# Kernel tuning notes

Hardware: AMD Instinct MI355X
Metric: run time of the kernel (lower is better)

Reference implementation:

```python
import jax, jax.numpy as jnp
import numpy as np

D = 128
N = 50000    # nodes in bond graph g
E = 500000   # edges in g == nodes in line graph lg
ELG = 500000 # edges in line graph lg


def _linear_params(key, d_in, d_out):
    k1, k2 = jax.random.split(key)
    s = 1.0 / np.sqrt(d_in)
    W = jax.random.uniform(k1, (d_in, d_out), jnp.float32, -s, s)
    b = jax.random.uniform(k2, (d_out,), jnp.float32, -s, s)
    return W, b


def setup_inputs() -> dict:
    key = jax.random.key(0)
    ks = jax.random.split(key, 32)
    inp = {
        'x': jax.random.normal(ks[0], (N, D), jnp.float32),
        'edge_x': jax.random.normal(ks[1], (E, D), jnp.float32),
        'lg_edge_attr': jax.random.normal(ks[2], (ELG, D), jnp.float32),
        'g_edge_index': jax.random.randint(ks[3], (2, E), 0, N),
        'lg_edge_index': jax.random.randint(ks[4], (2, ELG), 0, E),
    }
    i = 5
    for pre in ('eu', 'nu'):
        for nm in ('sg', 'dg', 'eg', 'su', 'du'):
            W, b = _linear_params(ks[i], D, D); i += 1
            inp[pre + '_W' + nm] = W
            inp[pre + '_b' + nm] = b
        inp[pre + '_gamma'] = jnp.ones((D,), jnp.float32)
        inp[pre + '_beta'] = jnp.zeros((D,), jnp.float32)
    return inp


def _layernorm(x, g, b):
    m = jnp.mean(x, -1, keepdims=True)
    v = jnp.var(x, -1, keepdims=True)
    return (x - m) * jax.lax.rsqrt(v + 1e-5) * g + b


def _egc(x, edge_index, edge_attr,
         Wsg, bsg, Wdg, bdg, Weg, beg, Wsu, bsu, Wdu, bdu, gamma, beta):
    # Edge-gated graph conv. PyG convention: x_i = x[dst], x_j = x[src],
    # aggregate messages at dst (edge_index[1]).
    src, dst = edge_index[0], edge_index[1]
    # Project once at node level, then gather (same math as gather-then-linear).
    sg = x @ Wsg + bsg          # src_gate(x_i) precomputed per node
    dg = x @ Wdg + bdg          # dst_gate(x_j)
    du = x @ Wdu + bdu          # dst_update(x_j)
    gate = jax.nn.silu(sg[dst] + dg[src] + edge_attr @ Weg + beg)  # [E, D]
    msg = gate * du[src]                                           # [E, D]
    aggr = jax.ops.segment_sum(msg, dst, num_segments=x.shape[0])  # [N, D]
    out = jax.nn.silu(_layernorm(x @ Wsu + bsu + aggr, gamma, beta))
    return out + x  # residual (in_channels == out_channels here)


def reference(x, edge_x, lg_edge_attr,
              eu_Wsg, eu_bsg, eu_Wdg, eu_bdg, eu_Weg, eu_beg,
              eu_Wsu, eu_bsu, eu_Wdu, eu_bdu, eu_gamma, eu_beta,
              nu_Wsg, nu_bsg, nu_Wdg, nu_bdg, nu_Weg, nu_beg,
              nu_Wsu, nu_bsu, nu_Wdu, nu_bdu, nu_gamma, nu_beta,
              g_edge_index, lg_edge_index):
    # 1) edge update on line graph (lg nodes are g's edges)
    ea = _egc(edge_x, lg_edge_index, lg_edge_attr,
              eu_Wsg, eu_bsg, eu_Wdg, eu_bdg, eu_Weg, eu_beg,
              eu_Wsu, eu_bsu, eu_Wdu, eu_bdu, eu_gamma, eu_beta)
    # 2) node update on bond graph using updated edge features
    xn = _egc(x, g_edge_index, ea,
              nu_Wsg, nu_bsg, nu_Wdg, nu_bdg, nu_Weg, nu_beg,
              nu_Wsu, nu_bsu, nu_Wdu, nu_bdu, nu_gamma, nu_beta)
    return (xn, ea)
```

## Files before the change

kernel.cpp:

```cpp
#include <hip/hip_runtime.h>
#include <stdint.h>

#define DD 128
#define WPAD 72

typedef __bf16 bf16x8 __attribute__((ext_vector_type(8)));
typedef float f32x4 __attribute__((ext_vector_type(4)));
typedef unsigned short u16;
typedef u16 u16x8 __attribute__((ext_vector_type(8)));

__device__ __forceinline__ u16 f2bf(float f) {
  union { __bf16 h; u16 u; } v; v.h = (__bf16)f; return v.u;
}
__device__ __forceinline__ float bf2f(u16 b) {
  union { uint32_t u; float f; } v; v.u = (uint32_t)b << 16; return v.f;
}
__device__ __forceinline__ float silu_f(float x) {
  return x / (1.0f + __expf(-x));
}
__device__ __forceinline__ uint32_t pkbf(float lo, float hi) {
  return (uint32_t)f2bf(lo) | ((uint32_t)f2bf(hi) << 16);
}

struct ARegs { f32x4 v[8][2]; };

__device__ __forceinline__ void issue_A(ARegs& r, const float* __restrict__ src,
                                        int base, int M, int tid) {
#pragma unroll
  for (int i = 0; i < 8; ++i) {
    int id = tid + (i << 8);
    int row = id >> 4;
    int cc = id & 15;
    if (base + row < M) {
      const f32x4* p = (const f32x4*)(src + (size_t)(base + row) * DD + cc * 8);
      r.v[i][0] = p[0];
      r.v[i][1] = p[1];
    } else {
      r.v[i][0] = (f32x4){0.f, 0.f, 0.f, 0.f};
      r.v[i][1] = (f32x4){0.f, 0.f, 0.f, 0.f};
    }
  }
}

__device__ __forceinline__ void write_A(u16* Ab, const ARegs& r, int tid) {
#pragma unroll
  for (int i = 0; i < 8; ++i) {
    int id = tid + (i << 8);
    int row = id >> 4;
    int cc = id & 15;
    u16x8 o;
    o[0] = f2bf(r.v[i][0][0]); o[1] = f2bf(r.v[i][0][1]);
    o[2] = f2bf(r.v[i][0][2]); o[3] = f2bf(r.v[i][0][3]);
    o[4] = f2bf(r.v[i][1][0]); o[5] = f2bf(r.v[i][1][1]);
    o[6] = f2bf(r.v[i][1][2]); o[7] = f2bf(r.v[i][1][3]);
    *(u16x8*)&Ab[row * DD + ((cc ^ (row & 7)) << 3)] = o;
  }
}

struct BRegs { bf16x8 b[4][4]; };

__device__ __forceinline__ void load_B(BRegs& br, const u16* __restrict__ wt,
                                       int lane, int wc) {
  int g = lane >> 4, r15 = lane & 15;
  const u16* wbase = wt + (size_t)(wc * 64 + r15) * DD;
#pragma unroll
  for (int kk = 0; kk < 4; ++kk) {
    int ko = ((kk << 2) | g) << 3;
#pragma unroll
    for (int n = 0; n < 4; ++n)
      br.b[kk][n] = *(const bf16x8*)&wbase[n * 16 * DD + ko];
  }
}

__device__ __forceinline__ void mma_stage(const u16* Ab, const BRegs& br,
                                          f32x4 acc[4][4], int lane, int wr) {
  int g = lane >> 4, r15 = lane & 15, s = r15 & 7;
#pragma unroll
  for (int kk = 0; kk < 4; ++kk) {
    bf16x8 af[4];
#pragma unroll
    for (int m = 0; m < 4; ++m) {
      int rr = wr * 64 + m * 16 + r15;
      af[m] = *(const bf16x8*)&Ab[rr * DD + ((((kk << 2) | g) ^ s) << 3)];
    }
#pragma unroll
    for (int m = 0; m < 4; ++m)
#pragma unroll
      for (int n = 0; n < 4; ++n)
        acc[m][n] = __builtin_amdgcn_mfma_f32_16x16x32_bf16(af[m], br.b[kk][n], acc[m][n], 0, 0, 0);
  }
}

__device__ __forceinline__ void init_acc(f32x4 a[4][4], const float* __restrict__ bias,
                                         int lane, int wc) {
  int l15 = lane & 15;
#pragma unroll
  for (int n = 0; n < 4; ++n) {
    float b = bias ? bias[wc * 64 + n * 16 + l15] : 0.f;
    f32x4 v = {b, b, b, b};
#pragma unroll
    for (int m = 0; m < 4; ++m) a[m][n] = v;
  }
}

__device__ __forceinline__ void store_lds_wave(const f32x4 acc[4][4], u16* wb,
                                               int lane) {
  int l15 = lane & 15;
  bool oddl = lane & 1;
#pragma unroll
  for (int m = 0; m < 4; ++m) {
    int rb = m * 16 + ((lane >> 4) << 2);
#pragma unroll
    for (int j = 0; j < 4; ++j) {
      int row = rb + j;
#pragma unroll
      for (int n0 = 0; n0 < 4; n0 += 2) {
        int c0 = n0 * 16 + l15;
        float v0 = acc[m][n0][j];
        float v1 = acc[m][n0 + 1][j];
        float t0 = __shfl_xor(v0, 1);
        float t1 = __shfl_xor(v1, 1);
        uint32_t pk = oddl ? pkbf(t1, v1) : pkbf(v0, t0);
        int col2 = oddl ? (c0 + 15) : c0;
        *(uint32_t*)&wb[row * WPAD + col2] = pk;
      }
    }
  }
}

__device__ __forceinline__ void copy_out_wave(const u16* wb, u16* __restrict__ out,
                                              size_t rs, int co, int base, int M,
                                              int lane, int wr, int wc,
                                              const int* sPerm) {
  int lr8 = lane >> 3;
  int lc = (lane & 7) * 8;
#pragma unroll
  for (int p = 0; p < 8; ++p) {
    int lrow = p * 8 + lr8;
    int row = wr * 64 + lrow;
    if (base + row < M) {
      int orow = sPerm ? sPerm[row] : (base + row);
      u16x8 v = *(const u16x8*)&wb[lrow * WPAD + lc];
      *(u16x8*)&out[(size_t)orow * rs + co + wc * 64 + lc] = v;
    }
  }
}

__device__ __forceinline__ void proj_four_body(
    int M, int base, const float* __restrict__ src, const u16* __restrict__ wt,
    const float* __restrict__ bF, u16* __restrict__ o_sg,
    u16* __restrict__ o_dgdu, u16* __restrict__ o_su, u16* Ab, u16* Wb) {
  int tid = threadIdx.x, lane = tid & 63, wid = tid >> 6;
  int wr = wid >> 1, wc = wid & 1;
  BRegs b0, b1;
  {
    ARegs ar;
    issue_A(ar, src, base, M, tid);
    load_B(b0, wt + 0 * 16384, lane, wc);
    write_A(Ab, ar, tid);
  }
  __syncthreads();
  u16* wb = Wb + wid * (64 * WPAD);
  f32x4 acc[4][4];
  init_acc(acc, bF, lane, wc);
  mma_stage(Ab, b0, acc, lane, wr);
  load_B(b1, wt + 1 * 16384, lane, wc);
  store_lds_wave(acc, wb, lane);
  copy_out_wave(wb, o_sg, DD, 0, base, M, lane, wr, wc, nullptr);
  init_acc(acc, nullptr, lane, wc);
  mma_stage(Ab, b1, acc, lane, wr);
  load_B(b0, wt + 3 * 16384, lane, wc);
  store_lds_wave(acc, wb, lane);
  copy_out_wave(wb, o_dgdu, 2 * DD, 0, base, M, lane, wr, wc, nullptr);
  init_acc(acc, bF + 128, lane, wc);
  mma_stage(Ab, b0, acc, lane, wr);
  load_B(b1, wt + 4 * 16384, lane, wc);
  store_lds_wave(acc, wb, lane);
  copy_out_wave(wb, o_dgdu, 2 * DD, DD, base, M, lane, wr, wc, nullptr);
  init_acc(acc, bF + 256, lane, wc);
  mma_stage(Ab, b1, acc, lane, wr);
  store_lds_wave(acc, wb, lane);
  copy_out_wave(wb, o_su, DD, 0, base, M, lane, wr, wc, nullptr);
}

__device__ __forceinline__ void proj_one_body(
    int M, int base, const float* __restrict__ src, const u16* __restrict__ wt,
    const int* __restrict__ perm, u16* __restrict__ o,
    u16* Ab, u16* Wb, int* sPerm) {
  int tid = threadIdx.x, lane = tid & 63, wid = tid >> 6;
  int wr = wid >> 1, wc = wid & 1;
  BRegs b0;
  {
    ARegs ar;
    issue_A(ar, src, base, M, tid);
    if (perm && tid < 128)
      sPerm[tid] = (base + tid < M) ? perm[base + tid] : 0;
    load_B(b0, wt, lane, wc);
    write_A(Ab, ar, tid);
  }
  __syncthreads();
  u16* wb = Wb + wid * (64 * WPAD);
  f32x4 acc[4][4];
  init_acc(acc, nullptr, lane, wc);
  mma_stage(Ab, b0, acc, lane, wr);
  store_lds_wave(acc, wb, lane);
  copy_out_wave(wb, o, DD, 0, base, M, lane, wr, wc, perm ? sPerm : nullptr);
}

__global__ void __launch_bounds__(256, 2) proj_mega(
    int gE, int gLG,
    int E, const float* __restrict__ ex, const u16* __restrict__ wtE,
    const float* __restrict__ bFE,
    u16* __restrict__ sgE, u16* __restrict__ dgduE, u16* __restrict__ suE,
    int ELG, const float* __restrict__ lga, const u16* __restrict__ wtLG,
    const int* __restrict__ permE, u16* __restrict__ egp,
    int N, const float* __restrict__ x, const u16* __restrict__ wtN,
    const float* __restrict__ bFN,
    u16* __restrict__ sgN, u16* __restrict__ dgduN, u16* __restrict__ suN) {
  __shared__ u16 Ab[128 * DD];
  __shared__ u16 Wb[4 * 64 * WPAD];
  __shared__ int sPerm[128];
  int b = blockIdx.x;
  if (b < gE)
    proj_four_body(E, b * 128, ex, wtE, bFE, sgE, dgduE, suE, Ab, Wb);
  else if (b < gE + gLG)
    proj_one_body(ELG, (b - gE) * 128, lga, wtLG, permE, egp, Ab, Wb, sPerm);
  else
    proj_four_body(N, (b - gE - gLG) * 128, x, wtN, bFN, sgN, dgduN, suN, Ab, Wb);
}

__global__ void __launch_bounds__(256, 2) proj_single(
    int M, const float* __restrict__ src, const u16* __restrict__ wt,
    const int* __restrict__ perm, u16* __restrict__ o) {
  __shared__ u16 Ab[128 * DD];
  __shared__ u16 Wb[4 * 64 * WPAD];
  __shared__ int sPerm[128];
  proj_one_body(M, blockIdx.x * 128, src, wt, perm, o, Ab, Wb, sPerm);
}

__global__ void __launch_bounds__(256) hist_kernel(const int* __restrict__ dst,
                                                   int Me, int* __restrict__ cnt) {
  int i = blockIdx.x * blockDim.x + threadIdx.x;
  if (i < Me) atomicAdd(&cnt[dst[i]], 1);
}

__global__ void __launch_bounds__(256) scan1_kernel(const int* __restrict__ cnt, int M,
                                                    int* __restrict__ out,
                                                    int* __restrict__ bsum) {
  __shared__ int sh[256];
  int t = threadIdx.x;
  int i0 = blockIdx.x * 1024 + t * 4;
  int v[4];
#pragma unroll
  for (int k = 0; k < 4; ++k) v[k] = (i0 + k < M) ? cnt[i0 + k] : 0;
  int s = v[0] + v[1] + v[2] + v[3];
  sh[t] = s;
  __syncthreads();
#pragma unroll
  for (int off = 1; off < 256; off <<= 1) {
    int x = (t >= off) ? sh[t - off] : 0;
    __syncthreads();
    sh[t] += x;
    __syncthreads();
  }
  int run = sh[t] - s;
  if (t == 255) bsum[blockIdx.x] = sh[255];
#pragma unroll
  for (int k = 0; k < 4; ++k) {
    if (i0 + k < M) out[i0 + k] = run;
    run += v[k];
  }
}

__global__ void __launch_bounds__(256) scan2_kernel(int* __restrict__ bsum, int NB) {
  __shared__ int sh[512];
  int t = threadIdx.x;
  for (int i = t; i < 512; i += 256) sh[i] = (i < NB) ? bsum[i] : 0;
  __syncthreads();
  for (int off = 1; off < 512; off <<= 1) {
    int tmp[2];
#pragma unroll
    for (int q = 0; q < 2; ++q) {
      int i = t + q * 256;
      tmp[q] = (i >= off) ? sh[i - off] : 0;
    }
    __syncthreads();
#pragma unroll
    for (int q = 0; q < 2; ++q) sh[t + q * 256] += tmp[q];
    __syncthreads();
  }
  for (int i = t; i < NB; i += 256) bsum[i] = (i == 0) ? 0 : sh[i - 1];
}

__global__ void __launch_bounds__(256) scan3_kernel(int* __restrict__ rowptr,
                                                    const int* __restrict__ bscan,
                                                    int M, int Medges,
                                                    int* __restrict__ head) {
  int i = blockIdx.x * blockDim.x + threadIdx.x;
  if (i < M) {
    int v = rowptr[i] + bscan[i >> 10];
    rowptr[i] = v;
    head[i] = v;
  }
  if (i == 0) rowptr[M] = Medges;
}

__global__ void __launch_bounds__(256) eid_kernel(const int* __restrict__ src,
                                                  const int* __restrict__ dst, int Me,
                                                  int* __restrict__ head,
                                                  int* __restrict__ srcs,
                                                  int* __restrict__ pos) {
  int i = blockIdx.x * blockDim.x + threadIdx.x;
  if (i < Me) {
    int s = atomicAdd(&head[dst[i]], 1);
    srcs[s] = src[i];
    pos[i] = s;
  }
}

__global__ void prep_weights(const float* __restrict__ w0, const float* __restrict__ w1,
                             const float* __restrict__ w2, const float* __restrict__ w3,
                             const float* __restrict__ w4, const float* __restrict__ w5,
                             const float* __restrict__ w6, const float* __restrict__ w7,
                             const float* __restrict__ w8, const float* __restrict__ w9,
                             u16* __restrict__ wt) {
  const float* W;
  switch (blockIdx.x) {
    case 0: W = w0; break; case 1: W = w1; break; case 2: W = w2; break;
    case 3: W = w3; break; case 4: W = w4; break; case 5: W = w5; break;
    case 6: W = w6; break; case 7: W = w7; break; case 8: W = w8; break;
    default: W = w9; break;
  }
  u16* dst = wt + blockIdx.x * 16384;
  for (int o = threadIdx.x; o < 16384; o += 256) {
    int n = o >> 7, k = o & 127;
    dst[o] = f2bf(W[k * DD + n]);
  }
}

__global__ void fold_bias(const float* __restrict__ e_sg, const float* __restrict__ e_dg,
                          const float* __restrict__ e_eg, const float* __restrict__ e_du,
                          const float* __restrict__ e_su,
                          const float* __restrict__ n_sg, const float* __restrict__ n_dg,
                          const float* __restrict__ n_eg, const float* __restrict__ n_du,
                          const float* __restrict__ n_su, float* __restrict__ out) {
  int i = threadIdx.x;
  if (i < 128) {
    out[i]        = e_sg[i] + e_dg[i] + e_eg[i];
    out[128 + i]  = e_du[i];
    out[256 + i]  = e_su[i];
    out[384 + i]  = n_sg[i] + n_dg[i] + n_eg[i];
    out[512 + i]  = n_du[i];
    out[640 + i]  = n_su[i];
  }
}

__global__ void __launch_bounds__(256) gfin_kernel(
    int M, const int* __restrict__ rptr,
    const int* __restrict__ srcs,
    const u16* __restrict__ sg_t, const u16* __restrict__ dgdu_t,
    const u16* __restrict__ su_t, const u16* __restrict__ egp,
    const float* __restrict__ gamma, const float* __restrict__ beta,
    const float* __restrict__ resid, float* __restrict__ out) {
  int gtid = blockIdx.x * blockDim.x + threadIdx.x;
  int r = gtid >> 4;
  int l16 = gtid & 15;
  if (r >= M) return;
  int c = l16 * 8;

  u16x8 sgp = *(const u16x8*)&sg_t[(size_t)r * DD + c];
  float sg[8], ax[8];
#pragma unroll
  for (int k = 0; k < 8; ++k) { sg[k] = bf2f(sgp[k]); ax[k] = 0.f; }

  int segb = rptr[r], sege = rptr[r + 1];
  for (int s = segb; s < sege; ++s) {
    int sv = srcs[s];
    u16x8 gp = *(const u16x8*)&egp[(size_t)s * DD + c];
    u16x8 dgp = *(const u16x8*)&dgdu_t[(size_t)sv * (2 * DD) + c];
    u16x8 dup = *(const u16x8*)&dgdu_t[(size_t)sv * (2 * DD) + DD + c];
#pragma unroll
    for (int k = 0; k < 8; ++k) {
      float g = silu_f(sg[k] + bf2f(dgp[k]) + bf2f(gp[k]));
      ax[k] += g * bf2f(dup[k]);
    }
  }

  u16x8 sup = *(const u16x8*)&su_t[(size_t)r * DD + c];
  float v[8];
  float sum = 0.f;
#pragma unroll
  for (int k = 0; k < 8; ++k) { v[k] = bf2f(sup[k]) + ax[k]; sum += v[k]; }
#pragma unroll
  for (int off = 1; off <= 8; off <<= 1) sum += __shfl_xor(sum, off);
  float mean = sum * (1.0f / 128.0f);
  float sq = 0.f;
#pragma unroll
  for (int k = 0; k < 8; ++k) { v[k] -= mean; sq += v[k] * v[k]; }
#pragma unroll
  for (int off = 1; off <= 8; off <<= 1) sq += __shfl_xor(sq, off);
  float rs = rsqrtf(sq * (1.0f / 128.0f) + 1e-5f);

  float4 gm0 = *(const float4*)&gamma[c];
  float4 gm1 = *(const float4*)&gamma[c + 4];
  float4 bt0 = *(const float4*)&beta[c];
  float4 bt1 = *(const float4*)&beta[c + 4];
  float4 rr0 = *(const float4*)&resid[(size_t)r * DD + c];
  float4 rr1 = *(const float4*)&resid[(size_t)r * DD + c + 4];
  float gmv[8] = {gm0.x, gm0.y, gm0.z, gm0.w, gm1.x, gm1.y, gm1.z, gm1.w};
  float btv[8] = {bt0.x, bt0.y, bt0.z, bt0.w, bt1.x, bt1.y, bt1.z, bt1.w};
  float rrv[8] = {rr0.x, rr0.y, rr0.z, rr0.w, rr1.x, rr1.y, rr1.z, rr1.w};
  float o[8];
#pragma unroll
  for (int k = 0; k < 8; ++k)
    o[k] = silu_f(v[k] * rs * gmv[k] + btv[k]) + rrv[k];
  float4 o0 = {o[0], o[1], o[2], o[3]};
  float4 o1 = {o[4], o[5], o[6], o[7]};
  *(float4*)&out[(size_t)r * DD + c] = o0;
  *(float4*)&out[(size_t)r * DD + c + 4] = o1;
}

extern "C" void kernel_launch(void* const* d_in, const int* in_sizes, int n_in,
                              void* d_out, int out_size, void* d_ws, size_t ws_size,
                              hipStream_t stream) {
  const float* x   = (const float*)d_in[0];
  const float* ex  = (const float*)d_in[1];
  const float* lga = (const float*)d_in[2];
  const int* gei   = (const int*)d_in[3];
  const int* lgei  = (const int*)d_in[4];
  int N   = in_sizes[0] / DD;
  int E   = in_sizes[3] / 2;
  int ELG = in_sizes[4] / 2;

  char* p = (char*)d_ws;
  size_t off = 0;
  auto alloc = [&](size_t bytes) { char* q = p + off; off += (bytes + 255) & ~255ull; return q; };

  u16* wt     = (u16*)alloc((size_t)10 * 16384 * 2);
  float* biasF = (float*)alloc(768 * 4);
  u16* sgE    = (u16*)alloc((size_t)E * DD * 2);
  u16* dgduE  = (u16*)alloc((size_t)E * 2 * DD * 2);
  u16* suE    = (u16*)alloc((size_t)E * DD * 2);
  int  maxME  = (ELG > E) ? ELG : E;
  u16* egpB   = (u16*)alloc((size_t)maxME * DD * 2);
  u16* sgN    = (u16*)alloc((size_t)N * DD * 2);
  u16* dgduN  = (u16*)alloc((size_t)N * 2 * DD * 2);
  u16* suN    = (u16*)alloc((size_t)N * DD * 2);
  int* cnt_e  = (int*)alloc((size_t)E * 4);
  int* rptr_e = (int*)alloc((size_t)(E + 1) * 4);
  int* head_e = (int*)alloc((size_t)E * 4);
  int* srcs_e = (int*)alloc((size_t)ELG * 4);
  int* pos_e  = (int*)alloc((size_t)ELG * 4);
  int* cnt_n  = (int*)alloc((size_t)N * 4);
  int* rptr_n = (int*)alloc((size_t)(N + 1) * 4);
  int* head_n = (int*)alloc((size_t)N * 4);
  int* srcs_n = (int*)alloc((size_t)E * 4);
  int* pos_n  = (int*)alloc((size_t)E * 4);
  int* bsum   = (int*)alloc(512 * 4);
  if (ws_size < off) return;

  float* xn_out = (float*)d_out;
  float* ea_out = (float*)d_out + (size_t)N * DD;

  prep_weights<<<10, 256, 0, stream>>>(
      (const float*)d_in[5], (const float*)d_in[7], (const float*)d_in[9],
      (const float*)d_in[13], (const float*)d_in[11],
      (const float*)d_in[17], (const float*)d_in[19], (const float*)d_in[21],
      (const float*)d_in[25], (const float*)d_in[23], wt);
  fold_bias<<<1, 128, 0, stream>>>(
      (const float*)d_in[6], (const float*)d_in[8], (const float*)d_in[10],
      (const float*)d_in[14], (const float*)d_in[12],
      (const float*)d_in[18], (const float*)d_in[20], (const float*)d_in[22],
      (const float*)d_in[26], (const float*)d_in[24], biasF);

  hipMemsetAsync(cnt_e, 0, (size_t)E * 4, stream);
  hipMemsetAsync(cnt_n, 0, (size_t)N * 4, stream);
  hist_kernel<<<(ELG + 255) / 256, 256, 0, stream>>>(lgei + ELG, ELG, cnt_e);
  hist_kernel<<<(E + 255) / 256, 256, 0, stream>>>(gei + E, E, cnt_n);

  int NBe = (E + 1023) / 1024;
  scan1_kernel<<<NBe, 256, 0, stream>>>(cnt_e, E, rptr_e, bsum);
  scan2_kernel<<<1, 256, 0, stream>>>(bsum, NBe);
  scan3_kernel<<<(E + 255) / 256, 256, 0, stream>>>(rptr_e, bsum, E, ELG, head_e);
  eid_kernel<<<(ELG + 255) / 256, 256, 0, stream>>>(lgei, lgei + ELG, ELG, head_e,
                                                    srcs_e, pos_e);

  int NBn = (N + 1023) / 1024;
  scan1_kernel<<<NBn, 256, 0, stream>>>(cnt_n, N, rptr_n, bsum);
  scan2_kernel<<<1, 256, 0, stream>>>(bsum, NBn);
  scan3_kernel<<<(N + 255) / 256, 256, 0, stream>>>(rptr_n, bsum, N, E, head_n);
  eid_kernel<<<(E + 255) / 256, 256, 0, stream>>>(gei, gei + E, E, head_n,
                                                  srcs_n, pos_n);

  int gE = (E + 127) / 128, gLG = (ELG + 127) / 128, gN = (N + 127) / 128;

  proj_mega<<<gE + gLG + gN, 256, 0, stream>>>(
      gE, gLG,
      E, ex, wt, biasF, sgE, dgduE, suE,
      ELG, lga, wt + 2 * 16384, pos_e, egpB,
      N, x, wt + 5 * 16384, biasF + 384, sgN, dgduN, suN);

  gfin_kernel<<<(E + 15) / 16, 256, 0, stream>>>(
      E, rptr_e, srcs_e, sgE, dgduE, suE, egpB,
      (const float*)d_in[15], (const float*)d_in[16], ex, ea_out);

  proj_single<<<gE, 256, 0, stream>>>(
      E, ea_out, wt + 7 * 16384, pos_n, egpB);
  gfin_kernel<<<(N + 15) / 16, 256, 0, stream>>>(
      N, rptr_n, srcs_n, sgN, dgduN, suN, egpB,
      (const float*)d_in[27], (const float*)d_in[28], x, xn_out);
}
```

Measured before the change: 809.0 us.

## Fuse node-graph edge-attr projection into line-graph gather/finalize kernel

The line-graph finalize kernel now also projects its freshly computed edge features through the node-update edge-gate weight with MFMA. It stages the bf16 row tile in shared memory and scatters results into a separate buffer ordered by the node-graph CSR. This removes the separate proj_single launch and the re-read of the fp32 ea output from global memory. In exchange it needs an extra E x 128 bf16 workspace buffer, and it adds shared memory, a block barrier and extra registers to a gather-bound kernel.

```diff
diff --git a/kernel.cpp b/kernel.cpp
--- a/kernel.cpp
+++ b/kernel.cpp
@@ -3,6 +3,7 @@
 
 #define DD 128
 #define WPAD 72
+#define EPAD 136
 
 typedef __bf16 bf16x8 __attribute__((ext_vector_type(8)));
 typedef float f32x4 __attribute__((ext_vector_type(4)));
@@ -355,69 +356,118 @@
   }
 }
 
+template <bool FUSE>
 __global__ void __launch_bounds__(256) gfin_kernel(
     int M, const int* __restrict__ rptr,
     const int* __restrict__ srcs,
     const u16* __restrict__ sg_t, const u16* __restrict__ dgdu_t,
     const u16* __restrict__ su_t, const u16* __restrict__ egp,
     const float* __restrict__ gamma, const float* __restrict__ beta,
-    const float* __restrict__ resid, float* __restrict__ out) {
-  int gtid = blockIdx.x * blockDim.x + threadIdx.x;
-  int r = gtid >> 4;
-  int l16 = gtid & 15;
-  if (r >= M) return;
+    const float* __restrict__ resid, float* __restrict__ out,
+    const u16* __restrict__ wtP, const int* __restrict__ posP,
+    u16* __restrict__ egp2) {
+  __shared__ u16 eaS[FUSE ? 16 * EPAD : 1];
+  __shared__ int sPos[FUSE ? 16 : 1];
+  int tid = threadIdx.x;
+  int rl = tid >> 4;
+  int l16 = tid & 15;
+  int r = blockIdx.x * 16 + rl;
   int c = l16 * 8;
-
-  u16x8 sgp = *(const u16x8*)&sg_t[(size_t)r * DD + c];
-  float sg[8], ax[8];
-#pragma unroll
-  for (int k = 0; k < 8; ++k) { sg[k] = bf2f(sgp[k]); ax[k] = 0.f; }
-
-  int segb = rptr[r], sege = rptr[r + 1];
-  for (int s = segb; s < sege; ++s) {
-    int sv = srcs[s];
-    u16x8 gp = *(const u16x8*)&egp[(size_t)s * DD + c];
-    u16x8 dgp = *(const u16x8*)&dgdu_t[(size_t)sv * (2 * DD) + c];
-    u16x8 dup = *(const u16x8*)&dgdu_t[(size_t)sv * (2 * DD) + DD + c];
-#pragma unroll
-    for (int k = 0; k < 8; ++k) {
-      float g = silu_f(sg[k] + bf2f(dgp[k]) + bf2f(gp[k]));
-      ax[k] += g * bf2f(dup[k]);
-    }
-  }
-
-  u16x8 sup = *(const u16x8*)&su_t[(size_t)r * DD + c];
-  float v[8];
-  float sum = 0.f;
-#pragma unroll
-  for (int k = 0; k < 8; ++k) { v[k] = bf2f(sup[k]) + ax[k]; sum += v[k]; }
-#pragma unroll
-  for (int off = 1; off <= 8; off <<= 1) sum += __shfl_xor(sum, off);
-  float mean = sum * (1.0f / 128.0f);
-  float sq = 0.f;
-#pragma unroll
-  for (int k = 0; k < 8; ++k) { v[k] -= mean; sq += v[k] * v[k]; }
-#pragma unroll
-  for (int off = 1; off <= 8; off <<= 1) sq += __shfl_xor(sq, off);
-  float rs = rsqrtf(sq * (1.0f / 128.0f) + 1e-5f);
-
-  float4 gm0 = *(const float4*)&gamma[c];
-  float4 gm1 = *(const float4*)&gamma[c + 4];
-  float4 bt0 = *(const float4*)&beta[c];
-  float4 bt1 = *(const float4*)&beta[c + 4];
-  float4 rr0 = *(const float4*)&resid[(size_t)r * DD + c];
-  float4 rr1 = *(const float4*)&resid[(size_t)r * DD + c + 4];
-  float gmv[8] = {gm0.x, gm0.y, gm0.z, gm0.w, gm1.x, gm1.y, gm1.z, gm1.w};
-  float btv[8] = {bt0.x, bt0.y, bt0.z, bt0.w, bt1.x, bt1.y, bt1.z, bt1.w};
-  float rrv[8] = {rr0.x, rr0.y, rr0.z, rr0.w, rr1.x, rr1.y, rr1.z, rr1.w};
+  bool act = (r < M);
+  if (!FUSE && !act) return;
+  if (FUSE && tid < 16)
+    sPos[tid] = (blockIdx.x * 16 + tid < M) ? posP[blockIdx.x * 16 + tid] : -1;
+
   float o[8];
-#pragma unroll
-  for (int k = 0; k < 8; ++k)
-    o[k] = silu_f(v[k] * rs * gmv[k] + btv[k]) + rrv[k];
-  float4 o0 = {o[0], o[1], o[2], o[3]};
-  float4 o1 = {o[4], o[5], o[6], o[7]};
-  *(float4*)&out[(size_t)r * DD + c] = o0;
-  *(float4*)&out[(size_t)r * DD + c + 4] = o1;
+  if (act) {
+    u16x8 sgp = *(const u16x8*)&sg_t[(size_t)r * DD + c];
+    float sg[8], ax[8];
+#pragma unroll
+    for (int k = 0; k < 8; ++k) { sg[k] = bf2f(sgp[k]); ax[k] = 0.f; }
+
+    int segb = rptr[r], sege = rptr[r + 1];
+    for (int s = segb; s < sege; ++s) {
+      int sv = srcs[s];
+      u16x8 gp = *(const u16x8*)&egp[(size_t)s * DD + c];
+      u16x8 dgp = *(const u16x8*)&dgdu_t[(size_t)sv * (2 * DD) + c];
+      u16x8 dup = *(const u16x8*)&dgdu_t[(size_t)sv * (2 * DD) + DD + c];
+#pragma unroll
+      for (int k = 0; k < 8; ++k) {
+        float g = silu_f(sg[k] + bf2f(dgp[k]) + bf2f(gp[k]));
+        ax[k] += g * bf2f(dup[k]);
+      }
+    }
+
+    u16x8 sup = *(const u16x8*)&su_t[(size_t)r * DD + c];
+    float v[8];
+    float sum = 0.f;
+#pragma unroll
+    for (int k = 0; k < 8; ++k) { v[k] = bf2f(sup[k]) + ax[k]; sum += v[k]; }
+#pragma unroll
+    for (int off = 1; off <= 8; off <<= 1) sum += __shfl_xor(sum, off);
+    float mean = sum * (1.0f / 128.0f);
+    float sq = 0.f;
+#pragma unroll
+    for (int k = 0; k < 8; ++k) { v[k] -= mean; sq += v[k] * v[k]; }
+#pragma unroll
+    for (int off = 1; off <= 8; off <<= 1) sq += __shfl_xor(sq, off);
+    float rs = rsqrtf(sq * (1.0f / 128.0f) + 1e-5f);
+
+    float4 gm0 = *(const float4*)&gamma[c];
+    float4 gm1 = *(const float4*)&gamma[c + 4];
+    float4 bt0 = *(const float4*)&beta[c];
+    float4 bt1 = *(const float4*)&beta[c + 4];
+    float4 rr0 = *(const float4*)&resid[(size_t)r * DD + c];
+    float4 rr1 = *(const float4*)&resid[(size_t)r * DD + c + 4];
+    float gmv[8] = {gm0.x, gm0.y, gm0.z, gm0.w, gm1.x, gm1.y, gm1.z, gm1.w};
+    float btv[8] = {bt0.x, bt0.y, bt0.z, bt0.w, bt1.x, bt1.y, bt1.z, bt1.w};
+    float rrv[8] = {rr0.x, rr0.y, rr0.z, rr0.w, rr1.x, rr1.y, rr1.z, rr1.w};
+#pragma unroll
+    for (int k = 0; k < 8; ++k)
+      o[k] = silu_f(v[k] * rs * gmv[k] + btv[k]) + rrv[k];
+    float4 o0 = {o[0], o[1], o[2], o[3]};
+    float4 o1 = {o[4], o[5], o[6], o[7]};
+    *(float4*)&out[(size_t)r * DD + c] = o0;
+    *(float4*)&out[(size_t)r * DD + c + 4] = o1;
+  }
+  if (!FUSE) return;
+
+  {
+    u16x8 e8;
+#pragma unroll
+    for (int k = 0; k < 8; ++k) e8[k] = act ? f2bf(o[k]) : (u16)0;
+    *(u16x8*)&eaS[rl * EPAD + c] = e8;
+    __syncthreads();
+
+    int lane = tid & 63, w = tid >> 6;
+    int g = lane >> 4, r15 = lane & 15;
+    f32x4 acc[2];
+    acc[0] = (f32x4){0.f, 0.f, 0.f, 0.f};
+    acc[1] = acc[0];
+#pragma unroll
+    for (int kk = 0; kk < 4; ++kk) {
+      int ko = ((kk << 2) | g) << 3;
+      bf16x8 af = *(const bf16x8*)&eaS[r15 * EPAD + ko];
+#pragma unroll
+      for (int n = 0; n < 2; ++n) {
+        bf16x8 bf = *(const bf16x8*)&wtP[(size_t)(w * 32 + n * 16 + r15) * DD + ko];
+        acc[n] = __builtin_amdgcn_mfma_f32_16x16x32_bf16(af, bf, acc[n], 0, 0, 0);
+      }
+    }
+    bool oddl = lane & 1;
+    int c0 = w * 32 + r15;
+#pragma unroll
+    for (int j = 0; j < 4; ++j) {
+      int row = ((lane >> 4) << 2) + j;
+      int porow = sPos[row];
+      float v0 = acc[0][j], v1 = acc[1][j];
+      float t0 = __shfl_xor(v0, 1);
+      float t1 = __shfl_xor(v1, 1);
+      uint32_t pk = oddl ? pkbf(t1, v1) : pkbf(v0, t0);
+      int col2 = oddl ? (c0 + 15) : c0;
+      if (porow >= 0) *(uint32_t*)&egp2[(size_t)porow * DD + col2] = pk;
+    }
+  }
 }
 
 extern "C" void kernel_launch(void* const* d_in, const int* in_sizes, int n_in,
@@ -459,6 +509,11 @@
   int* bsum   = (int*)alloc(512 * 4);
   if (ws_size < off) return;
 
+  size_t off_base = off;
+  u16* egp2 = (u16*)alloc((size_t)E * DD * 2);
+  bool fuse = (ws_size >= off);
+  if (!fuse) { off = off_base; egp2 = nullptr; }
+
   float* xn_out = (float*)d_out;
   float* ea_out = (float*)d_out + (size_t)N * DD;
 
@@ -500,13 +555,25 @@
       ELG, lga, wt + 2 * 16384, pos_e, egpB,
       N, x, wt + 5 * 16384, biasF + 384, sgN, dgduN, suN);
 
-  gfin_kernel<<<(E + 15) / 16, 256, 0, stream>>>(
-      E, rptr_e, srcs_e, sgE, dgduE, suE, egpB,
-      (const float*)d_in[15], (const float*)d_in[16], ex, ea_out);
-
-  proj_single<<<gE, 256, 0, stream>>>(
-      E, ea_out, wt + 7 * 16384, pos_n, egpB);
-  gfin_kernel<<<(N + 15) / 16, 256, 0, stream>>>(
-      N, rptr_n, srcs_n, sgN, dgduN, suN, egpB,
-      (const float*)d_in[27], (const float*)d_in[28], x, xn_out);
-}
+  if (fuse) {
+    gfin_kernel<true><<<(E + 15) / 16, 256, 0, stream>>>(
+        E, rptr_e, srcs_e, sgE, dgduE, suE, egpB,
+        (const float*)d_in[15], (const float*)d_in[16], ex, ea_out,
+        wt + 7 * 16384, pos_n, egp2);
+    gfin_kernel<false><<<(N + 15) / 16, 256, 0, stream>>>(
+        N, rptr_n, srcs_n, sgN, dgduN, suN, egp2,
+        (const float*)d_in[27], (const float*)d_in[28], x, xn_out,
+        nullptr, nullptr, nullptr);
+  } else {
+    gfin_kernel<false><<<(E + 15) / 16, 256, 0, stream>>>(
+        E, rptr_e, srcs_e, sgE, dgduE, suE, egpB,
+        (const float*)d_in[15], (const float*)d_in[16], ex, ea_out,
+        nullptr, nullptr, nullptr);
+    proj_single<<<gE, 256, 0, stream>>>(
+        E, ea_out, wt + 7 * 16384, pos_n, egpB);
+    gfin_kernel<false><<<(N + 15) / 16, 256, 0, stream>>>(
+        N, rptr_n, srcs_n, sgN, dgduN, suN, egpB,
+        (const float*)d_in[27], (const float*)d_in[28], x, xn_out,
+        nullptr, nullptr, nullptr);
+  }
+}
```

After: 868.3 us. 1.07x slower.
